# Kernel optimization log

Measured on AMD Instinct MI355X. Metric: run time of the kernel, lower is better.

Reference implementation:

```python
import jax, jax.numpy as jnp
import numpy as np

N, K, H, W = 2048, 8, 128, 128
G = 50              # glimpse size (50x50 from tem_rnn input 50*50)
ENC = 100           # glimpse encoder output (relation_rnn input arithmetic)
HID = 256
D_REL = ENC + (3 + 50) * 2 + HID          # 462
D_TEM = G * G + (3 + 50) * 2 + HID        # 2862


def _lin(k, out_d, in_d, scale=0.02):
    k1, k2 = jax.random.split(k)
    return (jax.random.normal(k1, (out_d, in_d), jnp.float32) * scale,
            jax.random.normal(k2, (out_d,), jnp.float32) * scale)


def _lstm_params(k, in_d, hid):
    k1, k2, k3, k4 = jax.random.split(k, 4)
    s = 0.02
    return (jax.random.normal(k1, (4 * hid, in_d), jnp.float32) * s,
            jax.random.normal(k2, (4 * hid, hid), jnp.float32) * s,
            jax.random.normal(k3, (4 * hid,), jnp.float32) * s,
            jax.random.normal(k4, (4 * hid,), jnp.float32) * s)


def lstm_cell(x, h, c, Wih, Whh, bih, bhh):
    g = x @ Wih.T + h @ Whh.T + (bih + bhh)
    i, f, gg, o = jnp.split(g, 4, axis=-1)
    i, f, o = jax.nn.sigmoid(i), jax.nn.sigmoid(f), jax.nn.sigmoid(o)
    c2 = f * c + i * jnp.tanh(gg)
    return o * jnp.tanh(c2), c2


def _bilinear_one(im, py, px):
    # im [H,W]; py,px [G,G] pixel coords; zeros padding like torch grid_sample
    x0 = jnp.floor(px); y0 = jnp.floor(py)
    wx1 = px - x0; wy1 = py - y0
    x0i = x0.astype(jnp.int32); y0i = y0.astype(jnp.int32)

    def gather(yi, xi):
        valid = (yi >= 0) & (yi < H) & (xi >= 0) & (xi < W)
        v = im[jnp.clip(yi, 0, H - 1), jnp.clip(xi, 0, W - 1)]
        return jnp.where(valid, v, 0.0)

    return ((1 - wy1) * (1 - wx1) * gather(y0i, x0i)
            + (1 - wy1) * wx1 * gather(y0i, x0i + 1)
            + wy1 * (1 - wx1) * gather(y0i + 1, x0i)
            + wy1 * wx1 * gather(y0i + 1, x0i + 1))


def stn_glimpse(z_where, img):
    # z_where [n,3] = (scale, tx, ty); theta = [[s,0,tx],[0,s,ty]] (attentive_stn_encode)
    s, tx, ty = z_where[:, 0], z_where[:, 1], z_where[:, 2]
    lin = jnp.linspace(-1.0, 1.0, G)
    gy, gx = jnp.meshgrid(lin, lin, indexing='ij')           # [G,G]
    px = (s[:, None, None] * gx + tx[:, None, None] + 1.0) * 0.5 * (W - 1)
    py = (s[:, None, None] * gy + ty[:, None, None] + 1.0) * 0.5 * (H - 1)
    out = jax.vmap(_bilinear_one)(img, py, px)               # [n,G,G]
    return out.reshape(out.shape[0], G * G)


def setup_inputs() -> dict:
    key = jax.random.key(0)
    ks = jax.random.split(key, 16)
    inp = {
        'img': jax.random.uniform(ks[0], (N, H, W), jnp.float32),
        'z_what_last': jax.random.normal(ks[1], (N, K, 50), jnp.float32),
        'z_where_last': jax.random.normal(ks[2], (N, K, 3), jnp.float32) * 0.3,
        'z_pres_last': jnp.ones((N, K, 1), jnp.float32),
        'hidden_last': jax.random.normal(ks[3], (N, K, HID), jnp.float32),
    }
    inp['W_loca'], inp['b_loca'] = _lin(ks[4], 3, HID)
    inp['Wg'], inp['bg'] = _lin(ks[5], ENC, G * G)
    (inp['Wih_rel'], inp['Whh_rel'], inp['bih_rel'], inp['bhh_rel']) = _lstm_params(ks[6], D_REL, HID)
    (inp['Wih_tem'], inp['Whh_tem'], inp['bih_tem'], inp['bhh_tem']) = _lstm_params(ks[7], D_TEM, HID)
    inp['Wm_wh'], inp['bm_wh'] = _lin(ks[8], 3, HID + 3)
    inp['Ws_wh'], inp['bs_wh'] = _lin(ks[9], 3, HID + 3)
    inp['Wm_wt'], inp['bm_wt'] = _lin(ks[10], 50, 50 + HID + HID)
    inp['Ws_wt'], inp['bs_wt'] = _lin(ks[11], 50, 50 + HID + HID)
    inp['Wm_pr'], inp['bm_pr'] = _lin(ks[12], 1, 50 + 3 + HID + HID)
    inp['Ws_pr'], inp['bs_pr'] = _lin(ks[13], 1, 50 + 3 + HID + HID)
    return inp


def reference(img, z_what_last, z_where_last, z_pres_last, hidden_last,
              W_loca, b_loca, Wg, bg,
              Wih_rel, Whh_rel, bih_rel, bhh_rel,
              Wih_tem, Whh_tem, bih_tem, bhh_tem,
              Wm_wh, bm_wh, Ws_wh, bs_wh,
              Wm_wt, bm_wt, Ws_wt, bs_wt,
              Wm_pr, bm_pr, Ws_pr, bs_pr):
    n = img.shape[0]

    def step(carry, xs):
        h_r, c_r, pzw, pzwhat = carry
        zwl, zwhatl, zpl, hl = xs   # [n,3],[n,50],[n,1],[n,256]
        # prop_loca: relu(linear(hidden)) + z_where_last
        zwb = jax.nn.relu(hl @ W_loca.T + b_loca) + zwl
        # STN glimpse + encode (bias pass)
        enc = jax.nn.relu(stn_glimpse(zwb, img) @ Wg.T + bg)        # [n,100]
        rin = jnp.concatenate([enc, zwl, pzw, zwhatl, pzwhat, hl], -1)  # [n,462]
        h_r2, c_r2 = lstm_cell(rin, h_r, c_r, Wih_rel, Whh_rel, bih_rel, bhh_rel)
        # z_where: latent predictor mean (eval mode)
        zw = jnp.concatenate([zwl, h_r2], -1) @ Wm_wh.T + bm_wh      # [n,3]
        # second STN glimpse with sampled where
        g2 = stn_glimpse(zw, img)                                    # [n,2500]
        tin = jnp.concatenate([g2, zw, pzw, zwhatl, pzwhat, hl], -1) # [n,2862]
        h_t, c_t = lstm_cell(tin, h_r2, c_r2, Wih_tem, Whh_tem, bih_tem, bhh_tem)
        # z_what mean
        zwhat = jnp.concatenate([zwhatl, h_r2, h_t], -1) @ Wm_wt.T + bm_wt  # [n,50]
        # z_pres: deterministic expectation of Bernoulli(mean*std) * previous pres
        zp_cal = jnp.concatenate([zwhat, zw, h_r2, h_t], -1)
        p = jax.nn.sigmoid(zp_cal @ Wm_pr.T + bm_pr) * jax.nn.sigmoid(zp_cal @ Ws_pr.T + bs_pr)
        zp = p * zpl                                                 # [n,1]
        return (h_r2, c_r2, zw, zwhat), (zwhat, zw, zp, h_t)

    carry0 = (jnp.zeros((n, HID), img.dtype), jnp.zeros((n, HID), img.dtype),
              jnp.zeros((n, 3), img.dtype), jnp.zeros((n, 50), img.dtype))
    xs = (jnp.swapaxes(z_where_last, 0, 1), jnp.swapaxes(z_what_last, 0, 1),
          jnp.swapaxes(z_pres_last, 0, 1), jnp.swapaxes(hidden_last, 0, 1))
    _, (zwhat_s, zw_s, zp_s, ht_s) = jax.lax.scan(step, carry0, xs)
    z_what = jnp.swapaxes(zwhat_s, 0, 1)   # [n,K,50]
    z_where = jnp.swapaxes(zw_s, 0, 1)     # [n,K,3]
    z_pres = jnp.swapaxes(zp_s, 0, 1)      # [n,K,1]
    h_temp = jnp.swapaxes(ht_s, 0, 1)      # [n,K,256]
    return z_what, z_where, z_pres, h_temp
```

## Files before the change

kernel.cpp:

```cpp
#include <hip/hip_runtime.h>
#include <hip/hip_bf16.h>
#include <math.h>

typedef __attribute__((ext_vector_type(8))) short bf16x8;
typedef __attribute__((ext_vector_type(4))) float f32x4;
using bf16 = __hip_bfloat16;

constexpr int NN   = 2048;
constexpr int KO   = 8;
constexpr int IH   = 128, IW = 128;
constexpr int GS   = 50;
constexpr int HIDD = 256;
constexpr int RIN_LD = 768;
constexpr int TIN_LD = 3136;
constexpr int G1_LD  = 2560;
constexpr int GROWS  = 64;
constexpr int GROWS2 = 48;

__device__ __forceinline__ float sigm(float x) { return 1.f/(1.f+expf(-x)); }

template<int OUT_BF16, int RELU>
__global__ __launch_bounds__(256, 2) void mfma_gemm(
    const bf16* __restrict__ A, int lda, int Kd,
    const bf16* __restrict__ Wt, int ldw, int M,
    const float* __restrict__ b1, const float* __restrict__ b2,
    void* __restrict__ Cout, int ldc, int nxb)
{
    __shared__ bf16x8 As16[512];
    __shared__ bf16x8 Bs16[512];
    const int b    = blockIdx.x;
    const int xcd  = b & 7;
    const int t    = b >> 3;
    const int n0   = (xcd + 8*(t / nxb))*64;
    const int m0   = (t % nxb)*64;
    const int tid  = threadIdx.x;
    const int wave = tid>>6, lane = tid&63;
    const int wy   = wave>>1, wx = wave&1;

    const int row = tid>>2, part = tid&3;
    const bf16* Ap = A + (size_t)(n0+row)*lda + part*8;
    const int   wm = m0 + row;
    const bool  wok = wm < M;
    const bf16* Wp = Wt + (size_t)(wok ? wm : 0)*ldw + part*8;
    const int dst0 = ((row>>4)*2+0)*64 + part*16 + (row&15);
    const int dst1 = dst0 + 64;

    f32x4 acc[2][2] = {};
    const bf16x8 z8 = {};
    bf16x8 pa0 = *(const bf16x8*)Ap;
    bf16x8 pa1 = *(const bf16x8*)(Ap + 32);
    bf16x8 pw0 = *(const bf16x8*)Wp;
    bf16x8 pw1 = *(const bf16x8*)(Wp + 32);

    for (int k0 = 0; k0 < Kd; k0 += 64) {
        __syncthreads();
        As16[dst0] = pa0;
        As16[dst1] = pa1;
        Bs16[dst0] = wok ? pw0 : z8;
        Bs16[dst1] = wok ? pw1 : z8;
        __syncthreads();
        if (k0 + 64 < Kd) {
            pa0 = *(const bf16x8*)(Ap + k0 + 64);
            pa1 = *(const bf16x8*)(Ap + k0 + 96);
            pw0 = *(const bf16x8*)(Wp + k0 + 64);
            pw1 = *(const bf16x8*)(Wp + k0 + 96);
        }
        bf16x8 av[2][2], bv[2][2];
        #pragma unroll
        for (int i=0;i<2;i++)
            #pragma unroll
            for (int h=0;h<2;h++) av[i][h] = As16[((wy*2+i)*2+h)*64 + lane];
        #pragma unroll
        for (int j=0;j<2;j++)
            #pragma unroll
            for (int h=0;h<2;h++) bv[j][h] = Bs16[((wx*2+j)*2+h)*64 + lane];
        #pragma unroll
        for (int h=0;h<2;h++)
            #pragma unroll
            for (int i=0;i<2;i++)
                #pragma unroll
                for (int j=0;j<2;j++)
                    acc[i][j] = __builtin_amdgcn_mfma_f32_16x16x32_bf16(av[i][h], bv[j][h], acc[i][j], 0, 0, 0);
    }

    const int q = lane>>4, r = lane&15;
    #pragma unroll
    for (int j=0;j<2;j++) {
        int col = m0 + wx*32 + j*16 + r;
        if (col < M) {
            float bias = 0.f;
            if (b1) bias += b1[col];
            if (b2) bias += b2[col];
            #pragma unroll
            for (int i=0;i<2;i++) {
                #pragma unroll
                for (int reg=0;reg<4;reg++) {
                    float v = acc[i][j][reg] + bias;
                    if (RELU) v = fmaxf(v, 0.f);
                    size_t idx = (size_t)(n0 + wy*32 + i*16 + q*4 + reg)*ldc + col;
                    if (OUT_BF16) ((bf16*)Cout)[idx] = __float2bfloat16(v);
                    else          ((float*)Cout)[idx] = v;
                }
            }
        }
    }
}

__device__ __forceinline__ void glimpse_points_global(const float* __restrict__ im,
                                                      float s, float tx, float ty,
                                                      bf16* __restrict__ drow) {
    const float GXS = 2.0f/49.0f;
    const float txp = tx + 1.0f, typ = ty + 1.0f;
    for (int p2 = threadIdx.x; p2 < 1250; p2 += 256) {
        int i = p2 / 25, j = (p2 - i*25)*2;
        float gy  = fmaf((float)i, GXS, -1.0f);
        float py  = fmaf(s, gy, typ)*63.5f;
        float y0f = floorf(py); float fy = py - y0f; int y0 = (int)y0f;
        float wy0 = ((unsigned)y0     < 128u) ? (1.f - fy) : 0.f;
        float wy1 = ((unsigned)(y0+1) < 128u) ? fy         : 0.f;
        const float* r0 = im + min(max(y0,  0),127)*IW;
        const float* r1 = im + min(max(y0+1,0),127)*IW;
        float gxa = fmaf((float)j, GXS, -1.0f);
        float pxa = fmaf(s, gxa, txp)*63.5f;
        float xa0f = floorf(pxa); float fa = pxa - xa0f; int xa0 = (int)xa0f;
        float wa0 = ((unsigned)xa0     < 128u) ? (1.f - fa) : 0.f;
        float wa1 = ((unsigned)(xa0+1) < 128u) ? fa         : 0.f;
        int xa0c = min(max(xa0,  0),127), xa1c = min(max(xa0+1,0),127);
        float gxb = fmaf((float)(j+1), GXS, -1.0f);
        float pxb = fmaf(s, gxb, txp)*63.5f;
        float xb0f = floorf(pxb); float fb = pxb - xb0f; int xb0 = (int)xb0f;
        float wb0 = ((unsigned)xb0     < 128u) ? (1.f - fb) : 0.f;
        float wb1 = ((unsigned)(xb0+1) < 128u) ? fb         : 0.f;
        int xb0c = min(max(xb0,  0),127), xb1c = min(max(xb0+1,0),127);

        float va = fmaf(wy1, fmaf(wa0, r1[xa0c], wa1*r1[xa1c]),
                   wy0 *     fmaf(wa0, r0[xa0c], wa1*r0[xa1c]));
        float vb = fmaf(wy1, fmaf(wb0, r1[xb0c], wb1*r1[xb1c]),
                   wy0 *     fmaf(wb0, r0[xb0c], wb1*r0[xb1c]));

        bf16 b0 = __float2bfloat16(va), b1 = __float2bfloat16(vb);
        unsigned short u0, u1;
        __builtin_memcpy(&u0, &b0, 2); __builtin_memcpy(&u1, &b1, 2);
        *(unsigned int*)(drow + i*GS + j) = (unsigned)u0 | ((unsigned)u1 << 16);
    }
}

__device__ __forceinline__ void glimpse_points_lds(const float* __restrict__ rows,
                                                   int ylo, int nrows,
                                                   float s, float tx, float ty,
                                                   bf16* __restrict__ drow) {
    const float GXS = 2.0f/49.0f;
    const float txp = tx + 1.0f, typ = ty + 1.0f;
    for (int p2 = threadIdx.x; p2 < 1250; p2 += 256) {
        int i = p2 / 25, j = (p2 - i*25)*2;
        float gy  = fmaf((float)i, GXS, -1.0f);
        float py  = fmaf(s, gy, typ)*63.5f;
        float y0f = floorf(py); float fy = py - y0f; int y0 = (int)y0f;
        float wy0 = ((unsigned)y0     < 128u) ? (1.f - fy) : 0.f;
        float wy1 = ((unsigned)(y0+1) < 128u) ? fy         : 0.f;
        const float* r0 = rows + min(max(y0-ylo,   0), nrows-1)*IW;
        const float* r1 = rows + min(max(y0+1-ylo, 0), nrows-1)*IW;
        float gxa = fmaf((float)j, GXS, -1.0f);
        float pxa = fmaf(s, gxa, txp)*63.5f;
        float xa0f = floorf(pxa); float fa = pxa - xa0f; int xa0 = (int)xa0f;
        float wa0 = ((unsigned)xa0     < 128u) ? (1.f - fa) : 0.f;
        float wa1 = ((unsigned)(xa0+1) < 128u) ? fa         : 0.f;
        int xa0c = min(max(xa0,  0),127), xa1c = min(max(xa0+1,0),127);
        float gxb = fmaf((float)(j+1), GXS, -1.0f);
        float pxb = fmaf(s, gxb, txp)*63.5f;
        float xb0f = floorf(pxb); float fb = pxb - xb0f; int xb0 = (int)xb0f;
        float wb0 = ((unsigned)xb0     < 128u) ? (1.f - fb) : 0.f;
        float wb1 = ((unsigned)(xb0+1) < 128u) ? fb         : 0.f;
        int xb0c = min(max(xb0,  0),127), xb1c = min(max(xb0+1,0),127);
        float va = fmaf(wy1, fmaf(wa0, r1[xa0c], wa1*r1[xa1c]),
                   wy0 *     fmaf(wa0, r0[xa0c], wa1*r0[xa1c]));
        float vb = fmaf(wy1, fmaf(wb0, r1[xb0c], wb1*r1[xb1c]),
                   wy0 *     fmaf(wb0, r0[xb0c], wb1*r0[xb1c]));
        bf16 b0 = __float2bfloat16(va), b1 = __float2bfloat16(vb);
        unsigned short u0, u1;
        __builtin_memcpy(&u0, &b0, 2); __builtin_memcpy(&u1, &b1, 2);
        *(unsigned int*)(drow + i*GS + j) = (unsigned)u0 | ((unsigned)u1 << 16);
    }
}

__global__ __launch_bounds__(256) void glimpse_batch(const float* __restrict__ img,
                                                     const float* __restrict__ z,
                                                     bf16* __restrict__ dst, int ldd,
                                                     bf16* __restrict__ rin,
                                                     const float* __restrict__ z_where_last,
                                                     const float* __restrict__ z_what_last,
                                                     const float* __restrict__ hidden_last,
                                                     int cbase) {
    __shared__ float rows[GROWS*IW];
    int b = blockIdx.x;
    int n = b & (NN-1);
    int sl = b >> 11;
    const float* im = img + (size_t)n*IH*IW;
    float s  = z[b*3+0];
    float tx = z[b*3+1];
    float ty = z[b*3+2];
    bf16* drow = dst + (size_t)b*ldd;

    const float txp = tx + 1.0f, typ = ty + 1.0f;
    float pyA = fmaf(s, -1.f, typ)*63.5f;
    float pyB = fmaf(s,  1.f, typ)*63.5f;
    int ylo = (int)floorf(fminf(pyA, pyB));
    int yhi = (int)floorf(fmaxf(pyA, pyB)) + 1;
    ylo = min(max(ylo, 0), 127);
    yhi = min(max(yhi, 0), 127);
    int nrows = yhi - ylo + 1;

    if (nrows <= GROWS) {
        const float4* src = (const float4*)(im + ylo*IW);
        float4* d4 = (float4*)rows;
        int tot = nrows*(IW/4);
        for (int t = threadIdx.x; t < tot; t += 256) d4[t] = src[t];
        __syncthreads();
        glimpse_points_lds(rows, ylo, nrows, s, tx, ty, drow);
    } else {
        glimpse_points_global(im, s, tx, ty, drow);
    }

    int k = cbase + sl;
    bf16* rrow = rin + (size_t)b*RIN_LD;
    for (int c = threadIdx.x; c < 309; c += 256) {
        float v; int col;
        if (c < 3)       { col = 100 + c;      v = z_where_last[((size_t)n*KO + k)*3 + c]; }
        else if (c < 53) { col = 106 + (c-3);  v = z_what_last[((size_t)n*KO + k)*50 + (c-3)]; }
        else             { col = 206 + (c-53); v = hidden_last[((size_t)n*KO + k)*HIDD + (c-53)]; }
        rrow[col] = __float2bfloat16(v);
    }
}

__global__ __launch_bounds__(256) void rel_glimpse2(
    const float* __restrict__ gates, float* __restrict__ h_r, float* __restrict__ c_r,
    const float* __restrict__ z_where_last,
    const float* __restrict__ Wm_wh, const float* __restrict__ bm_wh,
    float* __restrict__ zw_cur, float* __restrict__ out_zwhere,
    bf16* __restrict__ rin_next, bf16* __restrict__ tin,
    const float* __restrict__ img,
    const float* __restrict__ zw_prev, const float* __restrict__ zwhat_prev,
    const float* __restrict__ z_what_last, const float* __restrict__ hidden_last, int k)
{
    __shared__ float rows[GROWS2*IW];
    __shared__ float hs[256];
    __shared__ float zws[3];
    int n = blockIdx.x, j = threadIdx.x;
    const float* g = gates + (size_t)n*1024;
    float ig = sigm(g[j]);
    float fg = sigm(g[256+j]);
    float gg = tanhf(g[512+j]);
    float og = sigm(g[768+j]);
    int cidx = n*256 + j;
    float c2 = fg*c_r[cidx] + ig*gg;
    float hv = og*tanhf(c2);
    c_r[cidx] = c2;
    h_r[cidx] = hv;
    hs[j] = hv;
    bf16 hb = __float2bfloat16(hv);
    rin_next[(size_t)n*RIN_LD + 462 + j] = hb;
    bf16* trow = tin + (size_t)n*TIN_LD;
    trow[2862 + j] = hb;
    __syncthreads();
    int w = j >> 6, lane = j & 63;
    if (w < 3) {
        const float* wt = Wm_wh + w*259;
        float sa = 0.f;
        for (int i = lane; i < 256; i += 64) sa = fmaf(hs[i], wt[3+i], sa);
        #pragma unroll
        for (int off = 32; off; off >>= 1) sa += __shfl_down(sa, off);
        if (lane == 0) {
            const float* zwl = z_where_last + ((size_t)n*KO + k)*3;
            float acc = bm_wh[w] + sa;
            for (int i = 0; i < 3; i++) acc = fmaf(zwl[i], wt[i], acc);
            zws[w] = acc;
            zw_cur[n*3+w] = acc;
            out_zwhere[((size_t)n*KO + k)*3 + w] = acc;
            bf16 ab = __float2bfloat16(acc);
            rin_next[(size_t)n*RIN_LD + 103 + w] = ab;
            trow[2500 + w] = ab;
        }
    }
    __syncthreads();
    float s = zws[0], tx = zws[1], ty = zws[2];
    const float* im = img + (size_t)n*IH*IW;
    {
        const float typ = ty + 1.0f;
        float pyA = fmaf(s, -1.f, typ)*63.5f;
        float pyB = fmaf(s,  1.f, typ)*63.5f;
        int ylo = (int)floorf(fminf(pyA, pyB));
        int yhi = (int)floorf(fmaxf(pyA, pyB)) + 1;
        ylo = min(max(ylo, 0), 127);
        yhi = min(max(yhi, 0), 127);
        int nrows = yhi - ylo + 1;
        if (nrows <= GROWS2) {
            const float4* src = (const float4*)(im + ylo*IW);
            float4* d4 = (float4*)rows;
            int tot = nrows*(IW/4);
            for (int t = threadIdx.x; t < tot; t += 256) d4[t] = src[t];
            __syncthreads();
            glimpse_points_lds(rows, ylo, nrows, s, tx, ty, trow);
        } else {
            glimpse_points_global(im, s, tx, ty, trow);
        }
    }
    for (int c = 3 + j; c < 362; c += 256) {
        float v;
        if      (c <   6) v = zw_prev[n*3 + c-3];
        else if (c <  56) v = z_what_last[((size_t)n*KO + k)*50 + c-6];
        else if (c < 106) v = zwhat_prev[n*50 + c-56];
        else              v = hidden_last[((size_t)n*KO + k)*HIDD + c-106];
        trow[2500 + c] = __float2bfloat16(v);
    }
}

__global__ void zero_f32(float* __restrict__ p, int n) {
    int i = blockIdx.x*blockDim.x + threadIdx.x;
    if (i < n) p[i] = 0.f;
}

__global__ void repack_w(const float* __restrict__ s1, int K1,
                         const float* __restrict__ s2, int K2,
                         bf16* __restrict__ dst, int ldd, int M) {
    int gid = blockIdx.x*blockDim.x + threadIdx.x;
    if (gid >= M*ldd) return;
    int m = gid / ldd, c = gid - m*ldd;
    float v = 0.f;
    if (c < K1)           v = s1[(size_t)m*K1 + c];
    else if (c < K1+K2)   v = s2[(size_t)m*K2 + (c-K1)];
    dst[gid] = __float2bfloat16(v);
}

__global__ __launch_bounds__(256) void zwb_all_v2(const float* __restrict__ hidden_last,
                                                  const float* __restrict__ z_where_last,
                                                  const float* __restrict__ Wl, const float* __restrict__ bl,
                                                  float* __restrict__ zwb_all) {
    __shared__ float wls[768];
    for (int i = threadIdx.x; i < 768; i += 256) wls[i] = Wl[i];
    __syncthreads();
    int wv = threadIdx.x>>6, lane = threadIdx.x&63;
    int row = blockIdx.x*4 + wv;
    int s = row >> 11, n = row & (NN-1);
    const float* hl = hidden_last + ((size_t)n*KO + s)*HIDD;
    float4 h4 = *(const float4*)(hl + lane*4);
    float s0=0.f, s1=0.f, s2=0.f;
    #pragma unroll
    for (int r4=0;r4<4;r4++) {
        float hv = ((const float*)&h4)[r4];
        int i = lane*4 + r4;
        s0 = fmaf(hv, wls[i],     s0);
        s1 = fmaf(hv, wls[256+i], s1);
        s2 = fmaf(hv, wls[512+i], s2);
    }
    #pragma unroll
    for (int off=32; off; off>>=1) {
        s0 += __shfl_down(s0,off); s1 += __shfl_down(s1,off); s2 += __shfl_down(s2,off);
    }
    if (lane == 0) {
        const float* zwl = z_where_last + ((size_t)n*KO + s)*3;
        zwb_all[row*3+0] = fmaxf(s0+bl[0],0.f) + zwl[0];
        zwb_all[row*3+1] = fmaxf(s1+bl[1],0.f) + zwl[1];
        zwb_all[row*3+2] = fmaxf(s2+bl[2],0.f) + zwl[2];
    }
}

__global__ void zero_rin_carry(bf16* __restrict__ rin0) {
    int gid = blockIdx.x*blockDim.x + threadIdx.x;
    if (gid >= NN*309) return;
    int c = gid % 309, n = gid/309;
    int col = (c < 3) ? 103+c : ((c < 53) ? 156+(c-3) : 462+(c-53));
    rin0[(size_t)n*RIN_LD + col] = __float2bfloat16(0.f);
}

__global__ __launch_bounds__(256) void tem_fused(
    const float* __restrict__ gates, const float* __restrict__ c_r, const float* __restrict__ h_r,
    const float* __restrict__ z_what_last,
    const float* __restrict__ Wm_wt, const float* __restrict__ bm_wt,
    const float* __restrict__ Wm_pr, const float* __restrict__ bm_pr,
    const float* __restrict__ Ws_pr, const float* __restrict__ bs_pr,
    const float* __restrict__ zw_cur, const float* __restrict__ z_pres_last,
    float* __restrict__ zwhat_cur, float* __restrict__ out_zwhat,
    float* __restrict__ out_htemp, float* __restrict__ out_zpres,
    bf16* __restrict__ rin_next, int k)
{
    __shared__ float L[615];
    int n = blockIdx.x, j = threadIdx.x;
    const float* g = gates + (size_t)n*1024;
    float ig = sigm(g[j]);
    float fg = sigm(g[256+j]);
    float gg = tanhf(g[512+j]);
    float og = sigm(g[768+j]);
    float c2 = fg*c_r[n*256+j] + ig*gg;
    float hv = og*tanhf(c2);
    out_htemp[((size_t)n*KO + k)*HIDD + j] = hv;
    L[309+j] = hv;
    L[53+j]  = h_r[n*256+j];
    if (j < 50)      L[j]  = z_what_last[((size_t)n*KO + k)*50 + j];
    else if (j < 53) L[j]  = zw_cur[n*3 + (j-50)];
    __syncthreads();
    if (j < 200) {
        int m = j >> 2, part = j & 3;
        const float* wt = Wm_wt + m*562;
        float s = 0.f;
        for (int i = part; i < 562; i += 4) {
            float v = (i < 50) ? L[i] : L[i+3];
            s = fmaf(v, wt[i], s);
        }
        s += __shfl_down(s, 2);
        s += __shfl_down(s, 1);
        if (part == 0) {
            float acc = s + bm_wt[m];
            zwhat_cur[n*50+m] = acc;
            out_zwhat[((size_t)n*KO + k)*50 + m] = acc;
            rin_next[(size_t)n*RIN_LD + 156 + m] = __float2bfloat16(acc);
            L[565+m] = acc;
        }
    }
    __syncthreads();
    if (j < 64) {
        float s1 = 0.f, s2 = 0.f;
        for (int i = j; i < 565; i += 64) {
            float v = (i < 50) ? L[565+i] : L[i];
            s1 = fmaf(v, Wm_pr[i], s1);
            s2 = fmaf(v, Ws_pr[i], s2);
        }
        #pragma unroll
        for (int off = 32; off; off >>= 1) { s1 += __shfl_down(s1,off); s2 += __shfl_down(s2,off); }
        if (j == 0) {
            float p = sigm(s1 + bm_pr[0]) * sigm(s2 + bs_pr[0]);
            out_zpres[(size_t)n*KO + k] = p * z_pres_last[(size_t)n*KO + k];
        }
    }
}

extern "C" void kernel_launch(void* const* d_in, const int* in_sizes, int n_in,
                              void* d_out, int out_size, void* d_ws, size_t ws_size,
                              hipStream_t stream) {
    (void)in_sizes; (void)n_in; (void)out_size;
    const float* img          = (const float*)d_in[0];
    const float* z_what_last  = (const float*)d_in[1];
    const float* z_where_last = (const float*)d_in[2];
    const float* z_pres_last  = (const float*)d_in[3];
    const float* hidden_last  = (const float*)d_in[4];
    const float* W_loca = (const float*)d_in[5];
    const float* b_loca = (const float*)d_in[6];
    const float* Wg     = (const float*)d_in[7];
    const float* bg     = (const float*)d_in[8];
    const float* Wih_rel = (const float*)d_in[9];
    const float* Whh_rel = (const float*)d_in[10];
    const float* bih_rel = (const float*)d_in[11];
    const float* bhh_rel = (const float*)d_in[12];
    const float* Wih_tem = (const float*)d_in[13];
    const float* Whh_tem = (const float*)d_in[14];
    const float* bih_tem = (const float*)d_in[15];
    const float* bhh_tem = (const float*)d_in[16];
    const float* Wm_wh = (const float*)d_in[17];
    const float* bm_wh = (const float*)d_in[18];
    const float* Wm_wt = (const float*)d_in[21];
    const float* bm_wt = (const float*)d_in[22];
    const float* Wm_pr = (const float*)d_in[25];
    const float* bm_pr = (const float*)d_in[26];
    const float* Ws_pr = (const float*)d_in[27];
    const float* bs_pr = (const float*)d_in[28];

    char* base_p = (char*)d_ws;
    size_t off = 0;
    auto carve = [&](size_t bytes) -> char* {
        char* r = base_p + off;
        off += (bytes + 255) & ~(size_t)255;
        return r;
    };
    bf16*  tin      = (bf16*) carve((size_t)NN*TIN_LD*2);
    float* gates    = (float*)carve((size_t)NN*1024*4);
    bf16*  W_tem    = (bf16*) carve((size_t)1024*TIN_LD*2);
    bf16*  W_rel    = (bf16*) carve((size_t)1024*RIN_LD*2);
    bf16*  Wg_bf    = (bf16*) carve((size_t)100*G1_LD*2);
    float* zwb_all  = (float*)carve((size_t)KO*NN*3*4);
    float* h_r      = (float*)carve((size_t)NN*HIDD*4);
    float* c_r      = (float*)carve((size_t)NN*HIDD*4);
    float* zw1      = (float*)carve((size_t)NN*3*4);
    float* zwhat1   = (float*)carve((size_t)NN*50*4);
    float* zw0      = (float*)carve((size_t)NN*3*4);
    float* zwhat0   = (float*)carve((size_t)NN*50*4);
    size_t fixed_bytes = off;

    int CH = 1;
    for (int cand : {8, 4, 2}) {
        size_t need = fixed_bytes
                    + (((size_t)cand*NN*G1_LD*2 + 255) & ~(size_t)255)
                    + (((size_t)cand*NN*RIN_LD*2 + 255) & ~(size_t)255);
        if (need <= ws_size) { CH = cand; break; }
    }
    bf16* g1 = nullptr; int g1ld;
    bf16* rin;
    if (CH > 1) {
        g1   = (bf16*)carve((size_t)CH*NN*G1_LD*2);
        rin  = (bf16*)carve((size_t)CH*NN*RIN_LD*2);
        g1ld = G1_LD;
    } else {
        rin  = (bf16*)carve((size_t)NN*RIN_LD*2);
        g1   = tin;
        g1ld = TIN_LD;
    }

    float* out        = (float*)d_out;
    float* out_zwhat  = out;
    float* out_zwhere = out + (size_t)NN*KO*50;
    float* out_zpres  = out_zwhere + (size_t)NN*KO*3;
    float* out_htemp  = out_zpres + (size_t)NN*KO;

    {
        int nz = NN*(HIDD + 3 + 50);
        zero_f32<<<(nz+255)/256, 256, 0, stream>>>(c_r, nz);
    }
    zero_rin_carry<<<(NN*309+255)/256, 256, 0, stream>>>(rin);
    repack_w<<<((1024*RIN_LD)+255)/256, 256, 0, stream>>>(Wih_rel, 462, Whh_rel, 256, W_rel, RIN_LD, 1024);
    repack_w<<<((1024*TIN_LD)+255)/256, 256, 0, stream>>>(Wih_tem, 2862, Whh_tem, 256, W_tem, TIN_LD, 1024);
    repack_w<<<((100*G1_LD)+255)/256, 256, 0, stream>>>(Wg, 2500, nullptr, 0, Wg_bf, G1_LD, 100);
    zwb_all_v2<<<KO*NN/4, 256, 0, stream>>>(hidden_last, z_where_last, W_loca, b_loca, zwb_all);

    for (int cbase = 0; cbase < KO; cbase += CH) {
        glimpse_batch<<<CH*NN, 256, 0, stream>>>(img, zwb_all + (size_t)cbase*NN*3, g1, g1ld,
                                                 rin, z_where_last, z_what_last, hidden_last, cbase);
        mfma_gemm<1,1><<<2*CH*32, 256, 0, stream>>>(g1, g1ld, G1_LD, Wg_bf, G1_LD, 100, bg, nullptr, rin, RIN_LD, 2);

        for (int s = 0; s < CH; ++s) {
            int k = cbase + s;
            bf16* rin_k  = rin + (size_t)s*NN*RIN_LD;
            bf16* rin_nx = rin + (size_t)((s+1)%CH)*NN*RIN_LD;
            float* zw_cur     = (k & 1) ? zw1 : zw0;
            float* zw_prev    = (k & 1) ? zw0 : zw1;
            float* zwhat_cur  = (k & 1) ? zwhat1 : zwhat0;
            float* zwhat_prev = (k & 1) ? zwhat0 : zwhat1;

            mfma_gemm<0,0><<<512, 256, 0, stream>>>(rin_k, RIN_LD, RIN_LD, W_rel, RIN_LD, 1024, bih_rel, bhh_rel, gates, 1024, 16);
            rel_glimpse2<<<NN, 256, 0, stream>>>(gates, h_r, c_r, z_where_last, Wm_wh, bm_wh,
                                                 zw_cur, out_zwhere, rin_nx, tin,
                                                 img, zw_prev, zwhat_prev, z_what_last, hidden_last, k);
            mfma_gemm<0,0><<<512, 256, 0, stream>>>(tin, TIN_LD, TIN_LD, W_tem, TIN_LD, 1024, bih_tem, bhh_tem, gates, 1024, 16);
            tem_fused<<<NN, 256, 0, stream>>>(gates, c_r, h_r, z_what_last, Wm_wt, bm_wt, Wm_pr, bm_pr, Ws_pr, bs_pr,
                                              zw_cur, z_pres_last, zwhat_cur, out_zwhat, out_htemp, out_zpres, rin_nx, k);
        }
    }
}
```

Before: 1.328 ms.

## Double-buffer GEMM via direct global-to-LDS loads and split-K across two slices

Rewrites the MFMA GEMM to stage tiles directly from global memory into a double-buffered, XOR-swizzled LDS layout with global_load_lds, overlapping the next tile's load with current MFMAs. The LSTM gate GEMMs are split along K into two blockIdx.y slices writing separate partial gate buffers, which the consumer kernels sum before the activations. Occupancy hint rises to 4 blocks per CU. This is meant to hide load latency and double the block count for the 512-block GEMMs, at the cost of extra partial-sum traffic and larger LDS use. The swizzle only works if the direct-to-LDS lane ordering matches the computed pattern.

After: 1.198 ms. 9.8% less time.

```diff
diff --git a/kernel.cpp b/kernel.cpp
--- a/kernel.cpp
+++ b/kernel.cpp
@@ -20,60 +20,77 @@
 __device__ __forceinline__ float sigm(float x) { return 1.f/(1.f+expf(-x)); }
 
 template<int OUT_BF16, int RELU>
-__global__ __launch_bounds__(256, 2) void mfma_gemm(
-    const bf16* __restrict__ A, int lda, int Kd,
+__global__ __launch_bounds__(256, 4) void mfma_gemm(
+    const bf16* __restrict__ A, int lda, int Ktot,
     const bf16* __restrict__ Wt, int ldw, int M,
     const float* __restrict__ b1, const float* __restrict__ b2,
-    void* __restrict__ Cout, int ldc, int nxb)
+    void* __restrict__ Cout, int ldc, int nxb, int Kseg, int sstride)
 {
-    __shared__ bf16x8 As16[512];
-    __shared__ bf16x8 Bs16[512];
+    __shared__ __align__(16) bf16 As[2*4096];
+    __shared__ __align__(16) bf16 Bs[2*4096];
     const int b    = blockIdx.x;
     const int xcd  = b & 7;
     const int t    = b >> 3;
     const int n0   = (xcd + 8*(t / nxb))*64;
     const int m0   = (t % nxb)*64;
     const int tid  = threadIdx.x;
-    const int wave = tid>>6, lane = tid&63;
-    const int wy   = wave>>1, wx = wave&1;
-
-    const int row = tid>>2, part = tid&3;
-    const bf16* Ap = A + (size_t)(n0+row)*lda + part*8;
-    const int   wm = m0 + row;
-    const bool  wok = wm < M;
-    const bf16* Wp = Wt + (size_t)(wok ? wm : 0)*ldw + part*8;
-    const int dst0 = ((row>>4)*2+0)*64 + part*16 + (row&15);
-    const int dst1 = dst0 + 64;
+    const int w    = tid>>6, lane = tid&63;
+    const int wy   = w>>1, wx = w&1;
+    const int q    = lane>>4, fr = lane&15;
+
+    const int kbeg = blockIdx.y * Kseg;
+    const int kend = min(Ktot, kbeg + Kseg);
+    const int nk   = (kend - kbeg) >> 6;
+
+    const int r0   = tid>>3;
+    const int csrc = ((tid&7)*8) ^ ((r0&7)<<3);
+    const bf16* pa = A + (size_t)(n0 + r0)*lda + kbeg + csrc;
+    int wmr0 = m0 + r0;       if (wmr0 > M-1) wmr0 = M-1;
+    int wmr1 = m0 + r0 + 32;  if (wmr1 > M-1) wmr1 = M-1;
+    const bf16* pb  = Wt + (size_t)wmr0*ldw + kbeg + csrc;
+    const bf16* pb1 = Wt + (size_t)wmr1*ldw + kbeg + csrc;
 
     f32x4 acc[2][2] = {};
-    const bf16x8 z8 = {};
-    bf16x8 pa0 = *(const bf16x8*)Ap;
-    bf16x8 pa1 = *(const bf16x8*)(Ap + 32);
-    bf16x8 pw0 = *(const bf16x8*)Wp;
-    bf16x8 pw1 = *(const bf16x8*)(Wp + 32);
-
-    for (int k0 = 0; k0 < Kd; k0 += 64) {
-        __syncthreads();
-        As16[dst0] = pa0;
-        As16[dst1] = pa1;
-        Bs16[dst0] = wok ? pw0 : z8;
-        Bs16[dst1] = wok ? pw1 : z8;
-        __syncthreads();
-        if (k0 + 64 < Kd) {
-            pa0 = *(const bf16x8*)(Ap + k0 + 64);
-            pa1 = *(const bf16x8*)(Ap + k0 + 96);
-            pw0 = *(const bf16x8*)(Wp + k0 + 64);
-            pw1 = *(const bf16x8*)(Wp + k0 + 96);
-        }
+
+    auto stage = [&](int buf, int koff) {
+        bf16* la = As + buf*4096 + w*512;
+        bf16* lb = Bs + buf*4096 + w*512;
+        __builtin_amdgcn_global_load_lds(
+            (const __attribute__((address_space(1))) void*)(pa + koff),
+            (__attribute__((address_space(3))) void*)la, 16, 0, 0);
+        __builtin_amdgcn_global_load_lds(
+            (const __attribute__((address_space(1))) void*)(pa + koff + 32*(size_t)lda),
+            (__attribute__((address_space(3))) void*)(la + 2048), 16, 0, 0);
+        __builtin_amdgcn_global_load_lds(
+            (const __attribute__((address_space(1))) void*)(pb + koff),
+            (__attribute__((address_space(3))) void*)lb, 16, 0, 0);
+        __builtin_amdgcn_global_load_lds(
+            (const __attribute__((address_space(1))) void*)(pb1 + koff),
+            (__attribute__((address_space(3))) void*)(lb + 2048), 16, 0, 0);
+    };
+
+    stage(0, 0);
+    __syncthreads();
+    int cur = 0;
+    for (int kt = 0; kt < nk; ++kt) {
+        if (kt + 1 < nk) stage(cur ^ 1, (kt + 1) << 6);
+        const bf16* Ab = As + cur*4096;
+        const bf16* Bb = Bs + cur*4096;
         bf16x8 av[2][2], bv[2][2];
         #pragma unroll
-        for (int i=0;i<2;i++)
-            #pragma unroll
-            for (int h=0;h<2;h++) av[i][h] = As16[((wy*2+i)*2+h)*64 + lane];
+        for (int i=0;i<2;i++) {
+            int r = wy*32 + i*16 + fr;
+            int sw = (r&7)<<3, base = r*64;
+            av[i][0] = *(const bf16x8*)(Ab + base + ((q*8) ^ sw));
+            av[i][1] = *(const bf16x8*)(Ab + base + ((32 + q*8) ^ sw));
+        }
         #pragma unroll
-        for (int j=0;j<2;j++)
-            #pragma unroll
-            for (int h=0;h<2;h++) bv[j][h] = Bs16[((wx*2+j)*2+h)*64 + lane];
+        for (int j=0;j<2;j++) {
+            int r = wx*32 + j*16 + fr;
+            int sw = (r&7)<<3, base = r*64;
+            bv[j][0] = *(const bf16x8*)(Bb + base + ((q*8) ^ sw));
+            bv[j][1] = *(const bf16x8*)(Bb + base + ((32 + q*8) ^ sw));
+        }
         #pragma unroll
         for (int h=0;h<2;h++)
             #pragma unroll
@@ -81,16 +98,19 @@
                 #pragma unroll
                 for (int j=0;j<2;j++)
                     acc[i][j] = __builtin_amdgcn_mfma_f32_16x16x32_bf16(av[i][h], bv[j][h], acc[i][j], 0, 0, 0);
-    }
-
-    const int q = lane>>4, r = lane&15;
+        __syncthreads();
+        cur ^= 1;
+    }
+
     #pragma unroll
     for (int j=0;j<2;j++) {
-        int col = m0 + wx*32 + j*16 + r;
+        int col = m0 + wx*32 + j*16 + fr;
         if (col < M) {
             float bias = 0.f;
-            if (b1) bias += b1[col];
-            if (b2) bias += b2[col];
+            if (blockIdx.y == 0) {
+                if (b1) bias += b1[col];
+                if (b2) bias += b2[col];
+            }
             #pragma unroll
             for (int i=0;i<2;i++) {
                 #pragma unroll
@@ -99,7 +119,7 @@
                     if (RELU) v = fmaxf(v, 0.f);
                     size_t idx = (size_t)(n0 + wy*32 + i*16 + q*4 + reg)*ldc + col;
                     if (OUT_BF16) ((bf16*)Cout)[idx] = __float2bfloat16(v);
-                    else          ((float*)Cout)[idx] = v;
+                    else          ((float*)Cout)[(size_t)blockIdx.y*sstride + idx] = v;
                 }
             }
         }
@@ -201,7 +221,7 @@
     float ty = z[b*3+2];
     bf16* drow = dst + (size_t)b*ldd;
 
-    const float txp = tx + 1.0f, typ = ty + 1.0f;
+    const float typ = ty + 1.0f;
     float pyA = fmaf(s, -1.f, typ)*63.5f;
     float pyB = fmaf(s,  1.f, typ)*63.5f;
     int ylo = (int)floorf(fminf(pyA, pyB));
@@ -233,7 +253,8 @@
 }
 
 __global__ __launch_bounds__(256) void rel_glimpse2(
-    const float* __restrict__ gates, float* __restrict__ h_r, float* __restrict__ c_r,
+    const float* __restrict__ gates, const float* __restrict__ gates2,
+    float* __restrict__ h_r, float* __restrict__ c_r,
     const float* __restrict__ z_where_last,
     const float* __restrict__ Wm_wh, const float* __restrict__ bm_wh,
     float* __restrict__ zw_cur, float* __restrict__ out_zwhere,
@@ -246,11 +267,12 @@
     __shared__ float hs[256];
     __shared__ float zws[3];
     int n = blockIdx.x, j = threadIdx.x;
-    const float* g = gates + (size_t)n*1024;
-    float ig = sigm(g[j]);
-    float fg = sigm(g[256+j]);
-    float gg = tanhf(g[512+j]);
-    float og = sigm(g[768+j]);
+    const float* g  = gates  + (size_t)n*1024;
+    const float* g2 = gates2 + (size_t)n*1024;
+    float ig = sigm(g[j]       + g2[j]);
+    float fg = sigm(g[256+j]   + g2[256+j]);
+    float gg = tanhf(g[512+j]  + g2[512+j]);
+    float og = sigm(g[768+j]   + g2[768+j]);
     int cidx = n*256 + j;
     float c2 = fg*c_r[cidx] + ig*gg;
     float hv = og*tanhf(c2);
@@ -373,7 +395,8 @@
 }
 
 __global__ __launch_bounds__(256) void tem_fused(
-    const float* __restrict__ gates, const float* __restrict__ c_r, const float* __restrict__ h_r,
+    const float* __restrict__ gates, const float* __restrict__ gates2,
+    const float* __restrict__ c_r, const float* __restrict__ h_r,
     const float* __restrict__ z_what_last,
     const float* __restrict__ Wm_wt, const float* __restrict__ bm_wt,
     const float* __restrict__ Wm_pr, const float* __restrict__ bm_pr,
@@ -385,11 +408,12 @@
 {
     __shared__ float L[615];
     int n = blockIdx.x, j = threadIdx.x;
-    const float* g = gates + (size_t)n*1024;
-    float ig = sigm(g[j]);
-    float fg = sigm(g[256+j]);
-    float gg = tanhf(g[512+j]);
-    float og = sigm(g[768+j]);
+    const float* g  = gates  + (size_t)n*1024;
+    const float* g2 = gates2 + (size_t)n*1024;
+    float ig = sigm(g[j]       + g2[j]);
+    float fg = sigm(g[256+j]   + g2[256+j]);
+    float gg = tanhf(g[512+j]  + g2[512+j]);
+    float og = sigm(g[768+j]   + g2[768+j]);
     float c2 = fg*c_r[n*256+j] + ig*gg;
     float hv = og*tanhf(c2);
     out_htemp[((size_t)n*KO + k)*HIDD + j] = hv;
@@ -471,7 +495,7 @@
         return r;
     };
     bf16*  tin      = (bf16*) carve((size_t)NN*TIN_LD*2);
-    float* gates    = (float*)carve((size_t)NN*1024*4);
+    float* gates    = (float*)carve((size_t)2*NN*1024*4);
     bf16*  W_tem    = (bf16*) carve((size_t)1024*TIN_LD*2);
     bf16*  W_rel    = (bf16*) carve((size_t)1024*RIN_LD*2);
     bf16*  Wg_bf    = (bf16*) carve((size_t)100*G1_LD*2);
@@ -483,6 +507,7 @@
     float* zw0      = (float*)carve((size_t)NN*3*4);
     float* zwhat0   = (float*)carve((size_t)NN*50*4);
     size_t fixed_bytes = off;
+    float* gates2 = gates + (size_t)NN*1024;
 
     int CH = 1;
     for (int cand : {8, 4, 2}) {
@@ -519,10 +544,15 @@
     repack_w<<<((100*G1_LD)+255)/256, 256, 0, stream>>>(Wg, 2500, nullptr, 0, Wg_bf, G1_LD, 100);
     zwb_all_v2<<<KO*NN/4, 256, 0, stream>>>(hidden_last, z_where_last, W_loca, b_loca, zwb_all);
 
+    const int GSTR = NN*1024;
+    const int KSEG_REL = 384;
+    const int KSEG_TEM = 1600;
+
     for (int cbase = 0; cbase < KO; cbase += CH) {
         glimpse_batch<<<CH*NN, 256, 0, stream>>>(img, zwb_all + (size_t)cbase*NN*3, g1, g1ld,
                                                  rin, z_where_last, z_what_last, hidden_last, cbase);
-        mfma_gemm<1,1><<<2*CH*32, 256, 0, stream>>>(g1, g1ld, G1_LD, Wg_bf, G1_LD, 100, bg, nullptr, rin, RIN_LD, 2);
+        mfma_gemm<1,1><<<dim3(2*CH*32,1), 256, 0, stream>>>(g1, g1ld, G1_LD, Wg_bf, G1_LD, 100,
+                                                            bg, nullptr, rin, RIN_LD, 2, G1_LD, 0);
 
         for (int s = 0; s < CH; ++s) {
             int k = cbase + s;
@@ -533,12 +563,14 @@
             float* zwhat_cur  = (k & 1) ? zwhat1 : zwhat0;
             float* zwhat_prev = (k & 1) ? zwhat0 : zwhat1;
 
-            mfma_gemm<0,0><<<512, 256, 0, stream>>>(rin_k, RIN_LD, RIN_LD, W_rel, RIN_LD, 1024, bih_rel, bhh_rel, gates, 1024, 16);
-            rel_glimpse2<<<NN, 256, 0, stream>>>(gates, h_r, c_r, z_where_last, Wm_wh, bm_wh,
+            mfma_gemm<0,0><<<dim3(512,2), 256, 0, stream>>>(rin_k, RIN_LD, RIN_LD, W_rel, RIN_LD, 1024,
+                                                            bih_rel, bhh_rel, gates, 1024, 16, KSEG_REL, GSTR);
+            rel_glimpse2<<<NN, 256, 0, stream>>>(gates, gates2, h_r, c_r, z_where_last, Wm_wh, bm_wh,
                                                  zw_cur, out_zwhere, rin_nx, tin,
                                                  img, zw_prev, zwhat_prev, z_what_last, hidden_last, k);
-            mfma_gemm<0,0><<<512, 256, 0, stream>>>(tin, TIN_LD, TIN_LD, W_tem, TIN_LD, 1024, bih_tem, bhh_tem, gates, 1024, 16);
-            tem_fused<<<NN, 256, 0, stream>>>(gates, c_r, h_r, z_what_last, Wm_wt, bm_wt, Wm_pr, bm_pr, Ws_pr, bs_pr,
+            mfma_gemm<0,0><<<dim3(512,2), 256, 0, stream>>>(tin, TIN_LD, TIN_LD, W_tem, TIN_LD, 1024,
+                                                            bih_tem, bhh_tem, gates, 1024, 16, KSEG_TEM, GSTR);
+            tem_fused<<<NN, 256, 0, stream>>>(gates, gates2, c_r, h_r, z_what_last, Wm_wt, bm_wt, Wm_pr, bm_pr, Ws_pr, bs_pr,
                                               zw_cur, z_pres_last, zwhat_cur, out_zwhat, out_htemp, out_zpres, rin_nx, k);
         }
     }
```
